# Kernel tuning notes

Hardware: AMD Instinct MI355X
Metric: run time of the kernel (lower is better)

Reference implementation:

```python
import jax, jax.numpy as jnp
import numpy as np

H = 128  # GRU hidden dim

def gru_sequence(x_emb, W_ih, W_hh, b_ih, b_hh):
    """Run a GRU over x_emb (S, B, E); return final-step output (B, H).
    Matches torch.nn.GRU gate math:
      r = sig(W_ir x + b_ir + W_hr h + b_hr)
      z = sig(W_iz x + b_iz + W_hz h + b_hz)
      n = tanh(W_in x + b_in + r * (W_hn h + b_hn))
      h' = (1 - z) * n + z * h
    """
    S, B, E = x_emb.shape
    # Precompute input projections for all timesteps: (S, B, 3H)
    gx_all = jnp.einsum('sbe,ge->sbg', x_emb, W_ih) + b_ih

    def step(h, gx):
        gh = h @ W_hh.T + b_hh               # (B, 3H)
        r = jax.nn.sigmoid(gx[:, :H] + gh[:, :H])
        z = jax.nn.sigmoid(gx[:, H:2*H] + gh[:, H:2*H])
        n = jnp.tanh(gx[:, 2*H:] + r * gh[:, 2*H:])
        h_new = (1.0 - z) * n + z * h
        return h_new, None

    h0 = jnp.zeros((B, H), dtype=x_emb.dtype)
    h_final, _ = jax.lax.scan(step, h0, gx_all)
    return h_final  # (B, H) == out at last timestep


def setup_inputs() -> dict:
    key = jax.random.key(0)
    ks = jax.random.split(key, 12)
    S, B, V, E = 512, 512, 50000, 50
    x1 = jax.random.randint(ks[0], (S, B), 0, V, dtype=jnp.int32)
    x2 = jax.random.randint(ks[1], (S, B), 0, V, dtype=jnp.int32)
    emb = jax.random.uniform(ks[2], (V, E), jnp.float32, -0.01, 0.01)
    s = 1.0 / np.sqrt(H)
    W_ih = jax.random.uniform(ks[3], (3*H, E), jnp.float32, -s, s)
    W_hh = jax.random.uniform(ks[4], (3*H, H), jnp.float32, -s, s)
    b_ih = jax.random.uniform(ks[5], (3*H,), jnp.float32, -s, s)
    b_hh = jax.random.uniform(ks[6], (3*H,), jnp.float32, -s, s)
    s1 = 1.0 / np.sqrt(2*H)
    W1 = jax.random.uniform(ks[7], (H, 2*H), jnp.float32, -s1, s1)
    b1 = jax.random.uniform(ks[8], (H,), jnp.float32, -s1, s1)
    s2 = 1.0 / np.sqrt(H)
    W2 = jax.random.uniform(ks[9], (1, H), jnp.float32, -s2, s2)
    b2 = jax.random.uniform(ks[10], (1,), jnp.float32, -s2, s2)
    return {"x1": x1, "x2": x2, "emb": emb, "W_ih": W_ih, "W_hh": W_hh,
            "b_ih": b_ih, "b_hh": b_hh, "W1": W1, "b1": b1, "W2": W2, "b2": b2}


def reference(x1, x2, emb, W_ih, W_hh, b_ih, b_hh, W1, b1, W2, b2):
    e1 = emb[x1]  # (S, B, E)
    e2 = emb[x2]
    h1 = gru_sequence(e1, W_ih, W_hh, b_ih, b_hh)  # (B, H)
    h2 = gru_sequence(e2, W_ih, W_hh, b_ih, b_hh)  # (B, H)
    fc_in = jnp.concatenate([h1, h2], axis=-1)     # (B, 2H)
    hid = jax.nn.relu(fc_in @ W1.T + b1)
    out = jax.nn.sigmoid(hid @ W2.T + b2)          # (B, 1)
    return out
```

## Files before the change

### kernel.cpp

```cpp
#include <hip/hip_runtime.h>
#include <hip/hip_bf16.h>
#include <stdint.h>

#define S_LEN 512
#define BATCH 512
#define HID   128
#define G3    384
#define EMB   50
#define VOC   50000

#define NL2E  (-1.4426950408889634f)
#define N2L2E (-2.8853900817779268f)

typedef __attribute__((ext_vector_type(8))) short short8;
typedef __attribute__((ext_vector_type(4))) float float4v;
typedef __attribute__((ext_vector_type(2))) uint32_t uint2v;

__device__ inline unsigned short f2bf(float f) {
  union { float f; uint32_t u; } v; v.f = f;
  uint32_t u = v.u;
  u += 0x7fffu + ((u >> 16) & 1u);
  return (unsigned short)(u >> 16);
}
__device__ inline float bf2f(unsigned short h) {
  union { uint32_t u; float f; } v; v.u = ((uint32_t)h) << 16;
  return v.f;
}
__device__ inline uint32_t fbits(float f) {
  union { float f; uint32_t u; } v; v.f = f; return v.u;
}
__device__ inline float fast_sig(float x) {
  return __builtin_amdgcn_rcpf(1.f + __expf(-x));
}

__global__ __launch_bounds__(128) void prep_wih(
    const float* __restrict__ W_ih, const float* __restrict__ b_ih,
    const float* __restrict__ b_hh, unsigned short* __restrict__ wbf,
    float* __restrict__ sbias) {
  const int nt = blockIdx.x;
  const int kf = threadIdx.x >> 6;
  const int L  = threadIdx.x & 63;
  const int q = L >> 4, ln = L & 15;
  const int g = nt * 16 + ln;
  const float sc = (g < 256) ? NL2E : N2L2E;
  const int k0 = kf * 32 + q * 8;
  short8 v;
#pragma unroll
  for (int i = 0; i < 8; ++i) {
    const int k = k0 + i;
    v[i] = (k < EMB) ? (short)f2bf(W_ih[(size_t)g * EMB + k] * sc) : (short)0;
  }
  *(short8*)(wbf + (size_t)((nt * 2 + kf) * 64 + L) * 8) = v;
  if (threadIdx.x < 16) {
    const int gg = nt * 16 + threadIdx.x;
    const float s2 = (gg < 256) ? NL2E : N2L2E;
    sbias[gg] = s2 * (b_ih[gg] + (gg < 256 ? b_hh[gg] : 0.f));
  }
}

__global__ __launch_bounds__(256) void build_gxv(
    const float* __restrict__ emb, const unsigned short* __restrict__ wbf,
    const float* __restrict__ sbias, unsigned short* __restrict__ gxv) {
  __shared__ __align__(16) unsigned short cmat[64][392];
  const int w  = threadIdx.x >> 6;
  const int L  = threadIdx.x & 63;
  const int q  = L >> 4;
  const int ln = L & 15;
  const int vbase = blockIdx.x * 64 + w * 16;
  const int vloc  = w * 16;
  const int nblocks = (VOC + 63) / 64;

  const int vr = min(vbase + ln, VOC - 1);
  const float* arow = emb + (size_t)vr * EMB;
  short8 afr0, afr1;
  if (blockIdx.x != nblocks - 1) {
    const float4v x0 = *(const float4v*)(arow + q * 8);
    const float4v x1 = *(const float4v*)(arow + q * 8 + 4);
    const float4v y0 = *(const float4v*)(arow + 32 + q * 8);
    const float4v y1 = *(const float4v*)(arow + 32 + q * 8 + 4);
#pragma unroll
    for (int i = 0; i < 4; ++i) {
      afr0[i]     = (short)f2bf(x0[i]);
      afr0[i + 4] = (short)f2bf(x1[i]);
      const int ky0 = 32 + q * 8 + i, ky1 = ky0 + 4;
      afr1[i]     = (ky0 < EMB) ? (short)f2bf(y0[i]) : (short)0;
      afr1[i + 4] = (ky1 < EMB) ? (short)f2bf(y1[i]) : (short)0;
    }
  } else {
    float f;
#pragma unroll
    for (int i = 0; i < 8; ++i) {
      const int k = q * 8 + i; f = (k < EMB) ? arow[k] : 0.f;
      afr0[i] = (short)f2bf(f);
    }
#pragma unroll
    for (int i = 0; i < 8; ++i) {
      const int k = 32 + q * 8 + i; f = (k < EMB) ? arow[k] : 0.f;
      afr1[i] = (short)f2bf(f);
    }
  }

  short8 b0 = *(const short8*)(wbf + (size_t)(0 * 64 + L) * 8);
  short8 b1 = *(const short8*)(wbf + (size_t)(1 * 64 + L) * 8);
  float bias = sbias[ln];
  for (int nt = 0; nt < 24; ++nt) {
    short8 nb0, nb1; float nbias;
    if (nt < 23) {
      nb0 = *(const short8*)(wbf + (size_t)((nt * 2 + 2) * 64 + L) * 8);
      nb1 = *(const short8*)(wbf + (size_t)((nt * 2 + 3) * 64 + L) * 8);
      nbias = sbias[nt * 16 + 16 + ln];
    }
    const int gg = nt * 16 + ln;
    float4v acc = {bias, bias, bias, bias};
    acc = __builtin_amdgcn_mfma_f32_16x16x32_bf16(afr0, b0, acc, 0, 0, 0);
    acc = __builtin_amdgcn_mfma_f32_16x16x32_bf16(afr1, b1, acc, 0, 0, 0);
#pragma unroll
    for (int r = 0; r < 4; ++r)
      cmat[vloc + q * 4 + r][gg] = f2bf(acc[r]);
    b0 = nb0; b1 = nb1; bias = nbias;
  }
  __syncthreads();

  for (int idx = threadIdx.x; idx < 3072; idx += 256) {
    const int row = idx / 48, c8 = idx - row * 48;
    const int vrow = blockIdx.x * 64 + row;
    if (vrow < VOC) {
      short8 v = *(const short8*)(&cmat[row][c8 * 8]);
      *(short8*)(gxv + (size_t)vrow * G3 + c8 * 8) = v;
    }
  }
}

__global__ __launch_bounds__(512) void gru_kernel(
    const int* __restrict__ x1, const int* __restrict__ x2,
    const unsigned short* __restrict__ gxv, const float* __restrict__ W_hh,
    const float* __restrict__ b_hh, float* __restrict__ fcin) {
  const int bid   = blockIdx.x;
  const int gru   = bid >> 7;
  const int chunk = bid & 127;
  const int* xs   = gru ? x2 : x1;

  const int tid = threadIdx.x;
  const int w  = tid >> 6;
  const int L  = tid & 63;
  const int q  = L >> 4;
  const int ln = L & 15;
  const int jb = w * 16;
  const int g3 = ln >> 2;
  const int n  = ln & 3;
  const int j  = jb + q * 4 + g3;
  const int ng = chunk * 4 + n;

  __shared__ __align__(16) unsigned short hbuf[2][512];

  short8 afrag[3][4];
#pragma unroll
  for (int t = 0; t < 3; ++t) {
    const float sc = (t < 2) ? NL2E : N2L2E;
    const float* wr = W_hh + (size_t)(t * 128 + jb + ln) * HID;
#pragma unroll
    for (int kf = 0; kf < 4; ++kf) {
      const int k0 = kf * 32 + q * 8;
      float4v f0 = *(const float4v*)(wr + k0);
      float4v f1 = *(const float4v*)(wr + k0 + 4);
      short8 a;
#pragma unroll
      for (int i = 0; i < 4; ++i) a[i] = (short)f2bf(f0[i] * sc);
#pragma unroll
      for (int i = 0; i < 4; ++i) a[i + 4] = (short)f2bf(f1[i] * sc);
      afrag[t][kf] = a;
    }
  }

  float4v bhn4;
#pragma unroll
  for (int r = 0; r < 4; ++r) bhn4[r] = N2L2E * b_hh[2 * 128 + jb + q * 4 + r];

  for (int idx = tid; idx < 1024; idx += 512) ((unsigned short*)hbuf)[idx] = 0;

  float h = 0.f;

  unsigned short cr, cz, cn, mr, mz, mn;
  {
    const unsigned short* gp = gxv + (size_t)xs[ng] * G3;
    cr = gp[j]; cz = gp[128 + j]; cn = gp[256 + j];
    const unsigned short* gq = gxv + (size_t)xs[BATCH + ng] * G3;
    mr = gq[j]; mz = gq[128 + j]; mn = gq[256 + j];
  }
  int tokf = xs[2 * BATCH + ng];

  const int wofs = (((j >> 3) * 4 + n) << 3) + (j & 7);
  const int rofs = ((q * 4 + n) << 3);

  const bool selA = (ln & 4) != 0;
  const bool selB = (ln & 8) != 0;

  __syncthreads();

  for (int s = 0; s < S_LEN; ++s) {
    unsigned short fr, fz, fn;
    {
      const unsigned short* gp = gxv + (size_t)tokf * G3;
      fr = gp[j]; fz = gp[128 + j]; fn = gp[256 + j];
    }
    const int s3 = (s + 3 < S_LEN) ? (s + 3) : 0;
    const int tok3 = xs[s3 * BATCH + ng];

    const unsigned short* rb = hbuf[s & 1];
    short8 bfrag[4];
#pragma unroll
    for (int kf = 0; kf < 4; ++kf)
      bfrag[kf] = *(const short8*)(rb + kf * 128 + rofs);

    float vsel[3];
#pragma unroll
    for (int t = 0; t < 3; ++t) {
      float4v a0 = (t == 2) ? bhn4 : (float4v){0.f, 0.f, 0.f, 0.f};
      float4v a1 = {0.f, 0.f, 0.f, 0.f};
      a0 = __builtin_amdgcn_mfma_f32_16x16x32_bf16(afrag[t][0], bfrag[0], a0, 0, 0, 0);
      a1 = __builtin_amdgcn_mfma_f32_16x16x32_bf16(afrag[t][1], bfrag[1], a1, 0, 0, 0);
      a0 = __builtin_amdgcn_mfma_f32_16x16x32_bf16(afrag[t][2], bfrag[2], a0, 0, 0, 0);
      a1 = __builtin_amdgcn_mfma_f32_16x16x32_bf16(afrag[t][3], bfrag[3], a1, 0, 0, 0);
      const float4v acc = a0 + a1;
      const float x0 = selA ? acc[1] : acc[0];
      const float x1 = selA ? acc[3] : acc[2];
      vsel[t] = selB ? x1 : x0;
    }

    const float gr = bf2f(cr) + vsel[0];
    const float gz = bf2f(cz) + vsel[1];
    const float rg = __builtin_amdgcn_rcpf(1.f + __builtin_amdgcn_exp2f(gr));
    const float zg = __builtin_amdgcn_rcpf(1.f + __builtin_amdgcn_exp2f(gz));
    const float pre = bf2f(cn) + rg * vsel[2];
    const float sg  = __builtin_amdgcn_rcpf(1.f + __builtin_amdgcn_exp2f(pre));
    const float nn  = 2.f * sg - 1.f;
    h = zg * (h - nn) + nn;

    hbuf[(s + 1) & 1][wofs] = (unsigned short)((fbits(h) + 0x8000u) >> 16);

    asm volatile("s_waitcnt lgkmcnt(0)\n\ts_barrier" ::: "memory");

    cr = mr; cz = mz; cn = mn;
    mr = fr; mz = fz; mn = fn;
    tokf = tok3;
  }

  fcin[(size_t)ng * 256 + gru * 128 + j] = h;
}

__global__ __launch_bounds__(128) void head_kernel(
    const float* __restrict__ fcin, const float* __restrict__ W1,
    const float* __restrict__ b1, const float* __restrict__ W2,
    const float* __restrict__ b2, float* __restrict__ out) {
  __shared__ __align__(16) float fc[256];
  __shared__ float part[2];
  const int b = blockIdx.x, t = threadIdx.x;
  fc[t]       = fcin[(size_t)b * 256 + t];
  fc[t + 128] = fcin[(size_t)b * 256 + t + 128];
  __syncthreads();

  float acc = b1[t];
  const float4v* wr  = (const float4v*)(W1 + (size_t)t * 256);
  const float4v* fc4 = (const float4v*)fc;
#pragma unroll 8
  for (int k = 0; k < 64; ++k) {
    const float4v wv = wr[k];
    const float4v fv = fc4[k];
    acc += wv[0] * fv[0] + wv[1] * fv[1] + wv[2] * fv[2] + wv[3] * fv[3];
  }
  const float hid = fmaxf(acc, 0.f);

  float v = hid * W2[t];
#pragma unroll
  for (int o = 32; o > 0; o >>= 1) v += __shfl_xor(v, o, 64);
  if ((t & 63) == 0) part[t >> 6] = v;
  __syncthreads();
  if (t == 0) {
    const float s = part[0] + part[1] + b2[0];
    out[b] = fast_sig(s);
  }
}

extern "C" void kernel_launch(void* const* d_in, const int* in_sizes, int n_in,
                              void* d_out, int out_size, void* d_ws, size_t ws_size,
                              hipStream_t stream) {
  const int*   x1   = (const int*)d_in[0];
  const int*   x2   = (const int*)d_in[1];
  const float* emb  = (const float*)d_in[2];
  const float* W_ih = (const float*)d_in[3];
  const float* W_hh = (const float*)d_in[4];
  const float* b_ih = (const float*)d_in[5];
  const float* b_hh = (const float*)d_in[6];
  const float* W1   = (const float*)d_in[7];
  const float* b1   = (const float*)d_in[8];
  const float* W2   = (const float*)d_in[9];
  const float* b2   = (const float*)d_in[10];
  float* out = (float*)d_out;

  char* ws = (char*)d_ws;
  unsigned short* gxv  = (unsigned short*)ws;
  float*          fcin = (float*)(ws + (size_t)VOC * G3 * 2);
  unsigned short* wbf  = (unsigned short*)(ws + (size_t)VOC * G3 * 2 + 524288);
  float*          sbias= (float*)(ws + (size_t)VOC * G3 * 2 + 524288 + 49152);

  prep_wih<<<24, 128, 0, stream>>>(W_ih, b_ih, b_hh, wbf, sbias);
  build_gxv<<<(VOC + 63) / 64, 256, 0, stream>>>(emb, wbf, sbias, gxv);
  gru_kernel<<<256, 512, 0, stream>>>(x1, x2, gxv, W_hh, b_hh, fcin);
  head_kernel<<<512, 128, 0, stream>>>(fcin, W1, b1, W2, b2, out);
}
```

Measured before the change: 343.1 us.

## Fuse MLP head into GRU kernel via last-block-arrives atomic flag

Removes the separate head kernel launch. Each GRU block writes its final hidden state, then bumps a per-chunk atomic counter. The second of the two blocks (x1 and x2 GRUs) for a chunk computes the FC head for its 4 batch rows. The flags are zeroed in prep_wih. This saves a launch and its gap but adds fences and atomics, and the head work is serialized on the last-arriving blocks.

```diff
diff --git a/kernel.cpp b/kernel.cpp
--- a/kernel.cpp
+++ b/kernel.cpp
@@ -14,7 +14,6 @@
 
 typedef __attribute__((ext_vector_type(8))) short short8;
 typedef __attribute__((ext_vector_type(4))) float float4v;
-typedef __attribute__((ext_vector_type(2))) uint32_t uint2v;
 
 __device__ inline unsigned short f2bf(float f) {
   union { float f; uint32_t u; } v; v.f = f;
@@ -36,7 +35,7 @@
 __global__ __launch_bounds__(128) void prep_wih(
     const float* __restrict__ W_ih, const float* __restrict__ b_ih,
     const float* __restrict__ b_hh, unsigned short* __restrict__ wbf,
-    float* __restrict__ sbias) {
+    float* __restrict__ sbias, int* __restrict__ flags) {
   const int nt = blockIdx.x;
   const int kf = threadIdx.x >> 6;
   const int L  = threadIdx.x & 63;
@@ -56,6 +55,7 @@
     const float s2 = (gg < 256) ? NL2E : N2L2E;
     sbias[gg] = s2 * (b_ih[gg] + (gg < 256 ? b_hh[gg] : 0.f));
   }
+  if (nt == 0) flags[threadIdx.x] = 0;
 }
 
 __global__ __launch_bounds__(256) void build_gxv(
@@ -134,7 +134,10 @@
 __global__ __launch_bounds__(512) void gru_kernel(
     const int* __restrict__ x1, const int* __restrict__ x2,
     const unsigned short* __restrict__ gxv, const float* __restrict__ W_hh,
-    const float* __restrict__ b_hh, float* __restrict__ fcin) {
+    const float* __restrict__ b_hh, float* __restrict__ fcin,
+    int* __restrict__ flags, const float* __restrict__ W1,
+    const float* __restrict__ b1, const float* __restrict__ W2,
+    const float* __restrict__ b2, float* __restrict__ out) {
   const int bid   = blockIdx.x;
   const int gru   = bid >> 7;
   const int chunk = bid & 127;
@@ -246,22 +249,28 @@
   }
 
   fcin[(size_t)ng * 256 + gru * 128 + j] = h;
-}
-
-__global__ __launch_bounds__(128) void head_kernel(
-    const float* __restrict__ fcin, const float* __restrict__ W1,
-    const float* __restrict__ b1, const float* __restrict__ W2,
-    const float* __restrict__ b2, float* __restrict__ out) {
-  __shared__ __align__(16) float fc[256];
-  __shared__ float part[2];
-  const int b = blockIdx.x, t = threadIdx.x;
-  fc[t]       = fcin[(size_t)b * 256 + t];
-  fc[t + 128] = fcin[(size_t)b * 256 + t + 128];
-  __syncthreads();
-
-  float acc = b1[t];
-  const float4v* wr  = (const float4v*)(W1 + (size_t)t * 256);
-  const float4v* fc4 = (const float4v*)fc;
+
+  __shared__ int do_head;
+  __syncthreads();
+  if (tid == 0) {
+    __threadfence();
+    do_head = (atomicAdd(&flags[chunk], 1) == 1);
+  }
+  __syncthreads();
+  if (!do_head) return;
+  __threadfence();
+
+  __shared__ __align__(16) float fcs[4][256];
+  __shared__ float part[8];
+  for (int idx = tid; idx < 1024; idx += 512)
+    fcs[idx >> 8][idx & 255] = fcin[(size_t)(chunk * 4 + (idx >> 8)) * 256 + (idx & 255)];
+  __syncthreads();
+
+  const int bl = tid >> 7;
+  const int tt = tid & 127;
+  float acc = b1[tt];
+  const float4v* wr  = (const float4v*)(W1 + (size_t)tt * 256);
+  const float4v* fc4 = (const float4v*)fcs[bl];
 #pragma unroll 8
   for (int k = 0; k < 64; ++k) {
     const float4v wv = wr[k];
@@ -270,15 +279,13 @@
   }
   const float hid = fmaxf(acc, 0.f);
 
-  float v = hid * W2[t];
+  float v = hid * W2[tt];
 #pragma unroll
   for (int o = 32; o > 0; o >>= 1) v += __shfl_xor(v, o, 64);
-  if ((t & 63) == 0) part[t >> 6] = v;
-  __syncthreads();
-  if (t == 0) {
-    const float s = part[0] + part[1] + b2[0];
-    out[b] = fast_sig(s);
-  }
+  if ((tid & 63) == 0) part[tid >> 6] = v;
+  __syncthreads();
+  if (tt == 0)
+    out[chunk * 4 + bl] = fast_sig(part[2 * bl] + part[2 * bl + 1] + b2[0]);
 }
 
 extern "C" void kernel_launch(void* const* d_in, const int* in_sizes, int n_in,
@@ -302,9 +309,10 @@
   float*          fcin = (float*)(ws + (size_t)VOC * G3 * 2);
   unsigned short* wbf  = (unsigned short*)(ws + (size_t)VOC * G3 * 2 + 524288);
   float*          sbias= (float*)(ws + (size_t)VOC * G3 * 2 + 524288 + 49152);
-
-  prep_wih<<<24, 128, 0, stream>>>(W_ih, b_ih, b_hh, wbf, sbias);
+  int*            flags= (int*)(ws + (size_t)VOC * G3 * 2 + 524288 + 49152 + 1536);
+
+  prep_wih<<<24, 128, 0, stream>>>(W_ih, b_ih, b_hh, wbf, sbias, flags);
   build_gxv<<<(VOC + 63) / 64, 256, 0, stream>>>(emb, wbf, sbias, gxv);
-  gru_kernel<<<256, 512, 0, stream>>>(x1, x2, gxv, W_hh, b_hh, fcin);
-  head_kernel<<<512, 128, 0, stream>>>(fcin, W1, b1, W2, b2, out);
-}
+  gru_kernel<<<256, 512, 0, stream>>>(x1, x2, gxv, W_hh, b_hh, fcin,
+                                      flags, W1, b1, W2, b2, out);
+}
```

Result: slower. 366.9 us (+6.9%).
